# Optimization experiments

Measured on AMD Instinct MI355X. Metric: run time of the kernel, lower is better.

## Reference

```python
import jax, jax.numpy as jnp
import numpy as np

CLOUD_STDS = np.array([0.015, 0.015, 0.015], dtype=np.float32)
D_MODEL = 256
NHEAD = 8
NLAYERS = 4
DFF = 1024
K = 50
TEMP = 10000.0
ORIG_RES = 0.002
ENC_DIM = D_MODEL // 3 // 2  # 42
EPS = 1e-5


def setup_inputs() -> dict:
    key = jax.random.key(0)
    ks = jax.random.split(key, 10)
    B, F, S, d = 2, 8, 512, D_MODEL
    w = lambda k, shape: jax.random.normal(k, shape, jnp.float32) * 0.02
    return {
        "x": jax.random.normal(ks[0], (B, F, S, 3), jnp.float32),
        "is_pad": jnp.zeros((B, F, S), bool),
        "query_embed": w(ks[1], (1, d)),
        "Wq": w(ks[2], (NLAYERS, d, d)), "bq": jnp.zeros((NLAYERS, d), jnp.float32),
        "Wk": w(ks[3], (NLAYERS, d, d)), "bk": jnp.zeros((NLAYERS, d), jnp.float32),
        "Wv": w(ks[4], (NLAYERS, d, d)), "bv": jnp.zeros((NLAYERS, d), jnp.float32),
        "Wo": w(ks[5], (NLAYERS, d, d)), "bo": jnp.zeros((NLAYERS, d), jnp.float32),
        "ln1_g": jnp.ones((NLAYERS, d), jnp.float32), "ln1_b": jnp.zeros((NLAYERS, d), jnp.float32),
        "ln2_g": jnp.ones((NLAYERS, d), jnp.float32), "ln2_b": jnp.zeros((NLAYERS, d), jnp.float32),
        "W1": w(ks[6], (NLAYERS, d, DFF)), "b1": jnp.zeros((NLAYERS, DFF), jnp.float32),
        "W2": w(ks[7], (NLAYERS, DFF, d)), "b2": jnp.zeros((NLAYERS, d), jnp.float32),
    }


def _layer_norm(z, g, b):
    m = z.mean(-1, keepdims=True)
    v = ((z - m) ** 2).mean(-1, keepdims=True)
    return (z - m) / jnp.sqrt(v + EPS) * g + b


def reference(x, is_pad, query_embed, Wq, bq, Wk, bk, Wv, bv, Wo, bo,
              ln1_g, ln1_b, ln2_g, ln2_b, W1, b1, W2, b2):
    bin_size = jnp.asarray(ORIG_RES / CLOUD_STDS)  # (3,)
    B, F, S, _ = x.shape
    d = query_embed.shape[-1]
    H, dh = NHEAD, d // NHEAD
    S1 = S + 1

    def pos_encode(xb):  # (F,S,3) -> (F,S,d)
        xq = jnp.floor(xb / bin_size)  # torch float // == floor division
        dim_t = TEMP ** (jnp.arange(ENC_DIM, dtype=jnp.float32) / ENC_DIM)
        p = xq[..., None] / dim_t  # (F,S,3,E)
        pe = jnp.stack([jnp.sin(p), jnp.cos(p)], axis=-1).reshape(F, S, 3 * ENC_DIM * 2)
        pad = d - 6 * ENC_DIM  # left zero-pad (ZeroPad2d((pad,0,0,0)))
        return jnp.pad(pe, ((0, 0), (0, 0), (pad, 0)))

    def encode_one(xb, pb):  # xb:(F,S,3), pb:(F,S) bool
        # kNN mask: squared dists give same topk-smallest indices as cdist
        d2 = jnp.sum((xb[:, :, None, :] - xb[:, None, :, :]) ** 2, -1)  # (F,S,S)
        _, inds = jax.lax.top_k(-d2, K)  # (F,S,K)
        mask = jnp.ones((F, S1, S1), bool)  # True = disallowed
        fi = jnp.arange(F)[:, None, None]
        ci = jnp.arange(S)[None, :, None]
        mask = mask.at[fi, ci, inds].set(False)
        mask = mask.at[:, -1, :].set(False).at[:, :, -1].set(False)
        key_pad = jnp.concatenate([pb, jnp.zeros((F, 1), bool)], -1)  # (F,S1)
        bias = jnp.where(mask | key_pad[:, None, :], -1e9, 0.0).astype(jnp.float32)[:, None]  # (F,1,S1,S1)

        src = jnp.concatenate([pos_encode(xb), jnp.broadcast_to(query_embed, (F, 1, d))], axis=1)
        scale = 1.0 / jnp.sqrt(jnp.float32(dh))
        for l in range(NLAYERS):  # post-norm TransformerEncoderLayer
            q = (src @ Wq[l] + bq[l]).reshape(F, S1, H, dh)
            k = (src @ Wk[l] + bk[l]).reshape(F, S1, H, dh)
            v = (src @ Wv[l] + bv[l]).reshape(F, S1, H, dh)
            scores = jnp.einsum('fqhd,fkhd->fhqk', q, k) * scale + bias
            attn = jax.nn.softmax(scores, axis=-1)
            o = jnp.einsum('fhqk,fkhd->fqhd', attn, v).reshape(F, S1, d)
            src = _layer_norm(src + o @ Wo[l] + bo[l], ln1_g[l], ln1_b[l])
            ff = jax.nn.relu(src @ W1[l] + b1[l]) @ W2[l] + b2[l]
            src = _layer_norm(src + ff, ln2_g[l], ln2_b[l])
        return src[:, -1]  # query token encoding, (F,d)

    return jax.vmap(encode_one)(x, is_pad)  # (B,F,d)
```

## Files before the change

kernel.cpp:

```cpp
#include <hip/hip_runtime.h>
#include <math.h>

#define D 256
#define SS 512
#define S1 513
#define NC 16
#define NL 4
#define DFF_ 1024
#define NH 8
#define DH 32
#define KNN 50

typedef __attribute__((ext_vector_type(8))) short short8;
typedef __attribute__((ext_vector_type(4))) float float4v;
typedef __attribute__((address_space(1))) const void* gptr_t;
typedef __attribute__((address_space(3))) void* sptr_t;

__device__ __forceinline__ float b2f(short s) {
  return __uint_as_float(((unsigned)(unsigned short)s) << 16);
}
__device__ __forceinline__ short f2b(float f) {
  unsigned u = __float_as_uint(f);
  unsigned r = (u + 0x7fffu + ((u >> 16) & 1u)) >> 16;
  return (short)r;
}
__device__ __forceinline__ int mbcnt64(unsigned long long m) {
  return __builtin_amdgcn_mbcnt_hi((unsigned)(m >> 32),
         __builtin_amdgcn_mbcnt_lo((unsigned)m, 0));
}

__global__ __launch_bounds__(64) void posenc_kernel(const float* __restrict__ x,
    const float* __restrict__ qe, float* __restrict__ src, short* __restrict__ srcb) {
  int c = blockIdx.x, row = blockIdx.y, lane = threadIdx.x;
  size_t ro = ((size_t)c * S1 + row) * D;
  float* out = src + ro;
  short* outb = srcb + ro;
  if (row == SS) {
    for (int i = lane; i < D; i += 64) { float v = qe[i]; out[i] = v; outb[i] = f2b(v); }
    return;
  }
  const float* xp = x + ((size_t)c * SS + row) * 3;
  const float bin = (float)(0.002 / 0.015);
  float xq0 = floorf(xp[0] / bin);
  float xq1 = floorf(xp[1] / bin);
  float xq2 = floorf(xp[2] / bin);
  if (lane < 4) { out[lane] = 0.f; outb[lane] = 0; }
  for (int idx = lane; idx < 126; idx += 64) {
    int ch = idx / 42, e = idx - ch * 42;
    float dimt = powf(10000.0f, (float)e / 42.0f);
    float xq = (ch == 0) ? xq0 : ((ch == 1) ? xq1 : xq2);
    float p = xq / dimt;
    float sv = sinf(p), cv = cosf(p);
    int o0 = 4 + ch * 84 + e * 2;
    out[o0] = sv; out[o0 + 1] = cv;
    outb[o0] = f2b(sv); outb[o0 + 1] = f2b(cv);
  }
}

__global__ __launch_bounds__(64) void knn_kernel(const float* __restrict__ x, int* __restrict__ nbr) {
  int c = blockIdx.x, row = blockIdx.y, lane = threadIdx.x;
  const float* xc = x + (size_t)c * SS * 3;
  float px = xc[row * 3], py = xc[row * 3 + 1], pz = xc[row * 3 + 2];
  unsigned u[8];
  #pragma unroll
  for (int t = 0; t < 8; ++t) {
    int j = lane + 64 * t;
    float dx = px - xc[j * 3], dy = py - xc[j * 3 + 1], dz = pz - xc[j * 3 + 2];
    float s0 = __fmul_rn(dx, dx), s1 = __fmul_rn(dy, dy), s2 = __fmul_rn(dz, dz);
    u[t] = __float_as_uint(__fadd_rn(__fadd_rn(s0, s1), s2));
  }
  unsigned T = 0u;
  #pragma unroll 1
  for (int b = 30; b >= 0; --b) {
    unsigned cand = T | (1u << b);
    int cnt = 0;
    #pragma unroll
    for (int t = 0; t < 8; ++t) cnt += __popcll(__ballot(u[t] < cand));
    if (cnt < KNN) T = cand;
  }
  int L = 0;
  #pragma unroll
  for (int t = 0; t < 8; ++t) L += __popcll(__ballot(u[t] < T));
  int tneed = KNN - L;
  int wbase = 0;
  int* nrow = nbr + ((size_t)c * SS + row) * KNN;
  #pragma unroll
  for (int t = 0; t < 8; ++t) {
    bool less = u[t] < T;
    bool eq = u[t] == T;
    unsigned long long em = __ballot(eq);
    int myeq = mbcnt64(em);
    bool sel = eq && (myeq < tneed);
    bool win = less || sel;
    unsigned long long wm = __ballot(win);
    int mypos = wbase + mbcnt64(wm);
    if (win) nrow[mypos] = lane + 64 * t;
    wbase += __popcll(wm);
    int tie_take = __popcll(em); tie_take = tie_take < tneed ? tie_take : tneed;
    tneed -= tie_take;
  }
}

__global__ __launch_bounds__(256) void wconv4_kernel(const float* __restrict__ Wq,
    const float* __restrict__ Wk, const float* __restrict__ Wv, const float* __restrict__ Wo,
    short* __restrict__ Wqt, short* __restrict__ Wkt, short* __restrict__ Wvt, short* __restrict__ Wot) {
  __shared__ float t[32][33];
  int z = blockIdx.z, which = z >> 2, l = z & 3;
  const float* W = (which == 0 ? Wq : which == 1 ? Wk : which == 2 ? Wv : Wo) + (size_t)l * D * D;
  short* Wt = (which == 0 ? Wqt : which == 1 ? Wkt : which == 2 ? Wvt : Wot) + (size_t)l * D * D;
  int k0 = blockIdx.x * 32, n0 = blockIdx.y * 32;
  int tx = threadIdx.x, ty = threadIdx.y;
  #pragma unroll
  for (int i = 0; i < 4; ++i)
    t[ty + 8 * i][tx] = W[(size_t)(k0 + ty + 8 * i) * D + n0 + tx];
  __syncthreads();
  #pragma unroll
  for (int i = 0; i < 4; ++i)
    Wt[(size_t)(n0 + ty + 8 * i) * D + k0 + tx] = f2b(t[tx][ty + 8 * i]);
}

__global__ __launch_bounds__(256) void wconv_kernel(const float* __restrict__ W,
    short* __restrict__ Wt, int K, int N) {
  __shared__ float t[32][33];
  int m = blockIdx.z;
  const float* Wm = W + (size_t)m * K * N;
  short* Wtm = Wt + (size_t)m * K * N;
  int k0 = blockIdx.x * 32, n0 = blockIdx.y * 32;
  int tx = threadIdx.x, ty = threadIdx.y;
  #pragma unroll
  for (int i = 0; i < 4; ++i)
    t[ty + 8 * i][tx] = Wm[(size_t)(k0 + ty + 8 * i) * N + n0 + tx];
  __syncthreads();
  #pragma unroll
  for (int i = 0; i < 4; ++i)
    Wtm[(size_t)(n0 + ty + 8 * i) * K + k0 + tx] = f2b(t[tx][ty + 8 * i]);
}

template<typename OutT, int RELU>
__global__ __launch_bounds__(256) void mfma_gemm(
    const short* __restrict__ A,
    const short* __restrict__ B0, const short* __restrict__ B1, const short* __restrict__ B2,
    const float* __restrict__ bias0, const float* __restrict__ bias1, const float* __restrict__ bias2,
    OutT* __restrict__ C0, OutT* __restrict__ C1, OutT* __restrict__ C2,
    int M, int N, int Kd) {
  __shared__ short lds[16384];
  const short* Bt  = blockIdx.z == 0 ? B0 : (blockIdx.z == 1 ? B1 : B2);
  const float* bias = blockIdx.z == 0 ? bias0 : (blockIdx.z == 1 ? bias1 : bias2);
  OutT* C          = blockIdx.z == 0 ? C0 : (blockIdx.z == 1 ? C1 : C2);
  int bm = blockIdx.x * 128, bn = blockIdx.y * 128;
  int tid = threadIdx.x, lane = tid & 63, wid = tid >> 6;
  int wr = wid >> 1, wc = wid & 1;
  float4v acc[4][4];
  #pragma unroll
  for (int i = 0; i < 4; ++i)
    #pragma unroll
    for (int j = 0; j < 4; ++j) acc[i][j] = {0.f, 0.f, 0.f, 0.f};

  for (int k0 = 0; k0 < Kd; k0 += 64) {
    #pragma unroll
    for (int q = 0; q < 4; ++q) {
      int row = wid * 32 + q * 8 + (lane >> 3);
      int slot = lane & 7;
      int kofs = k0 + ((slot ^ (row & 7)) << 3);
      {
        int gr = bm + row; if (gr > M - 1) gr = M - 1;
        const short* gp = A + (size_t)gr * Kd + kofs;
        __builtin_amdgcn_global_load_lds((gptr_t)gp, (sptr_t)(&lds[(wid * 32 + q * 8) * 64]), 16, 0, 0);
      }
      {
        const short* gp = Bt + (size_t)(bn + row) * Kd + kofs;
        __builtin_amdgcn_global_load_lds((gptr_t)gp, (sptr_t)(&lds[8192 + (wid * 32 + q * 8) * 64]), 16, 0, 0);
      }
    }
    __syncthreads();
    #pragma unroll
    for (int kh = 0; kh < 2; ++kh) {
      short8 af[4], bf[4];
      int kk = kh * 4 + (lane >> 4);
      #pragma unroll
      for (int i = 0; i < 4; ++i) {
        int row = wr * 64 + i * 16 + (lane & 15);
        af[i] = *(const short8*)&lds[row * 64 + ((kk ^ (row & 7)) << 3)];
      }
      #pragma unroll
      for (int j = 0; j < 4; ++j) {
        int row = wc * 64 + j * 16 + (lane & 15);
        bf[j] = *(const short8*)&lds[8192 + row * 64 + ((kk ^ (row & 7)) << 3)];
      }
      #pragma unroll
      for (int i = 0; i < 4; ++i)
        #pragma unroll
        for (int j = 0; j < 4; ++j)
          acc[i][j] = __builtin_amdgcn_mfma_f32_16x16x32_bf16(af[i], bf[j], acc[i][j], 0, 0, 0);
    }
    __syncthreads();
  }
  #pragma unroll
  for (int i = 0; i < 4; ++i) {
    int gm0 = bm + wr * 64 + i * 16 + ((lane >> 4) << 2);
    #pragma unroll
    for (int j = 0; j < 4; ++j) {
      int gn = bn + wc * 64 + j * 16 + (lane & 15);
      float bsv = bias[gn];
      #pragma unroll
      for (int r = 0; r < 4; ++r) {
        int gm = gm0 + r;
        if (gm < M) {
          float v = acc[i][j][r] + bsv;
          if (RELU) v = fmaxf(v, 0.f);
          if constexpr (sizeof(OutT) == 2) C[(size_t)gm * N + gn] = f2b(v);
          else C[(size_t)gm * N + gn] = v;
        }
      }
    }
  }
}

__global__ __launch_bounds__(256) void gemm_ln(
    const short* __restrict__ A, const short* __restrict__ Bt,
    const float* __restrict__ bias, float* __restrict__ src, short* __restrict__ srcb,
    const float* __restrict__ g, const float* __restrict__ bb, int M, int Kd) {
  __shared__ short ldsA[64 * 64];
  __shared__ short ldsB[256 * 64];
  __shared__ float sBias[256], sG[256], sBb[256];
  int tid = threadIdx.x, lane = tid & 63, wid = tid >> 6;
  int bm = blockIdx.x * 64;
  sBias[tid] = bias[tid]; sG[tid] = g[tid]; sBb[tid] = bb[tid];
  float4v acc[16];
  #pragma unroll
  for (int j = 0; j < 16; ++j) acc[j] = {0.f, 0.f, 0.f, 0.f};

  for (int k0 = 0; k0 < Kd; k0 += 64) {
    int slot = lane & 7;
    #pragma unroll
    for (int q = 0; q < 2; ++q) {
      int row = q * 32 + wid * 8 + (lane >> 3);
      int kofs = k0 + ((slot ^ (row & 7)) << 3);
      int gr = bm + row; if (gr > M - 1) gr = M - 1;
      __builtin_amdgcn_global_load_lds((gptr_t)(A + (size_t)gr * Kd + kofs),
          (sptr_t)(&ldsA[(q * 32 + wid * 8) * 64]), 16, 0, 0);
    }
    #pragma unroll
    for (int q = 0; q < 8; ++q) {
      int row = q * 32 + wid * 8 + (lane >> 3);
      int kofs = k0 + ((slot ^ (row & 7)) << 3);
      __builtin_amdgcn_global_load_lds((gptr_t)(Bt + (size_t)row * Kd + kofs),
          (sptr_t)(&ldsB[(q * 32 + wid * 8) * 64]), 16, 0, 0);
    }
    __syncthreads();
    #pragma unroll
    for (int kh = 0; kh < 2; ++kh) {
      int kk = kh * 4 + (lane >> 4);
      int arow = wid * 16 + (lane & 15);
      short8 af = *(const short8*)&ldsA[arow * 64 + ((kk ^ (arow & 7)) << 3)];
      #pragma unroll
      for (int j = 0; j < 16; ++j) {
        int brow = j * 16 + (lane & 15);
        short8 bf = *(const short8*)&ldsB[brow * 64 + ((kk ^ (brow & 7)) << 3)];
        acc[j] = __builtin_amdgcn_mfma_f32_16x16x32_bf16(af, bf, acc[j], 0, 0, 0);
      }
    }
    __syncthreads();
  }
  int rowg = lane >> 4, coll = lane & 15;
  float z[16][4];
  #pragma unroll
  for (int j = 0; j < 16; ++j) {
    int gn = j * 16 + coll;
    float bsv = sBias[gn];
    #pragma unroll
    for (int r = 0; r < 4; ++r) {
      int gm = bm + wid * 16 + rowg * 4 + r;
      int gmc = gm < M ? gm : M - 1;
      z[j][r] = acc[j][r] + bsv + src[(size_t)gmc * D + gn];
    }
  }
  #pragma unroll
  for (int r = 0; r < 4; ++r) {
    float s = 0.f;
    #pragma unroll
    for (int j = 0; j < 16; ++j) s += z[j][r];
    s += __shfl_xor(s, 1); s += __shfl_xor(s, 2); s += __shfl_xor(s, 4); s += __shfl_xor(s, 8);
    float mean = s * (1.f / 256.f);
    float v = 0.f;
    #pragma unroll
    for (int j = 0; j < 16; ++j) { float d = z[j][r] - mean; v += d * d; }
    v += __shfl_xor(v, 1); v += __shfl_xor(v, 2); v += __shfl_xor(v, 4); v += __shfl_xor(v, 8);
    float scl = rsqrtf(v * (1.f / 256.f) + 1e-5f);
    int gm = bm + wid * 16 + rowg * 4 + r;
    if (gm < M) {
      #pragma unroll
      for (int j = 0; j < 16; ++j) {
        int gn = j * 16 + coll;
        float o = (z[j][r] - mean) * scl * sG[gn] + sBb[gn];
        src[(size_t)gm * D + gn] = o;
        srcb[(size_t)gm * D + gn] = f2b(o);
      }
    }
  }
}

__global__ __launch_bounds__(256) void attn_kernel2(const short* __restrict__ qb,
    const short* __restrict__ kb, const short* __restrict__ vb,
    const int* __restrict__ nbr, short* __restrict__ ob) {
  __shared__ float ps[S1 + 7];
  __shared__ float red[8];
  __shared__ float accp[8][32];
  __shared__ float sum_sh;
  int c = blockIdx.y;
  const float scale = 0.17677669529663687f;

  if (blockIdx.x < 128) {
    int lane = threadIdx.x & 63, w = threadIdx.x >> 6;
    int qrow = blockIdx.x * 4 + w;
    int h = lane >> 3, j = lane & 7;
    const short* cb_k = kb + (size_t)c * S1 * D;
    const short* cb_v = vb + (size_t)c * S1 * D;
    float qv[32];
    {
      const short* qp = qb + ((size_t)c * S1 + qrow) * D + h * DH;
      #pragma unroll
      for (int d8 = 0; d8 < 4; ++d8) {
        short8 q8 = *(const short8*)(qp + d8 * 8);
        #pragma unroll
        for (int e = 0; e < 8; ++e) qv[d8 * 8 + e] = b2f(q8[e]);
      }
    }
    int idxr = SS;
    if (lane < KNN) idxr = nbr[((size_t)c * SS + qrow) * KNN + lane];
    float p[7];
    float mx = -INFINITY;
    #pragma unroll
    for (int c7 = 0; c7 < 7; ++c7) {
      int slot = c7 * 8 + j;
      int is = __shfl(idxr, slot);
      const short* kp = cb_k + (size_t)is * D + h * DH;
      float a = 0.f;
      #pragma unroll
      for (int d8 = 0; d8 < 4; ++d8) {
        short8 k8 = *(const short8*)(kp + d8 * 8);
        #pragma unroll
        for (int e = 0; e < 8; ++e) a += qv[d8 * 8 + e] * b2f(k8[e]);
      }
      p[c7] = (slot < 51) ? a * scale : -INFINITY;
      mx = fmaxf(mx, p[c7]);
    }
    #pragma unroll
    for (int o = 1; o < 8; o <<= 1) mx = fmaxf(mx, __shfl_xor(mx, o));
    float sum = 0.f;
    #pragma unroll
    for (int c7 = 0; c7 < 7; ++c7) { p[c7] = expf(p[c7] - mx); sum += p[c7]; }
    #pragma unroll
    for (int o = 1; o < 8; o <<= 1) sum += __shfl_xor(sum, o);
    float acc0 = 0.f, acc1 = 0.f, acc2 = 0.f, acc3 = 0.f;
    #pragma unroll
    for (int t = 0; t < 51; ++t) {
      float pp = __shfl(p[t >> 3], h * 8 + (t & 7));
      int is = __shfl(idxr, t);
      const short* vp = cb_v + (size_t)is * D + h * DH + j * 4;
      int2 v2 = *(const int2*)vp;
      acc0 += pp * __uint_as_float((unsigned)v2.x << 16);
      acc1 += pp * __uint_as_float((unsigned)v2.x & 0xffff0000u);
      acc2 += pp * __uint_as_float((unsigned)v2.y << 16);
      acc3 += pp * __uint_as_float((unsigned)v2.y & 0xffff0000u);
    }
    float inv = 1.0f / sum;
    short* op = ob + ((size_t)c * S1 + qrow) * D + h * DH + j * 4;
    short4 o4;
    o4.x = f2b(acc0 * inv); o4.y = f2b(acc1 * inv);
    o4.z = f2b(acc2 * inv); o4.w = f2b(acc3 * inv);
    *(short4*)op = o4;
  } else {
    int tid = threadIdx.x, lane = tid & 63, w = tid >> 6;
    int h = blockIdx.x - 128;
    const short* qp = qb + ((size_t)c * S1 + SS) * D + h * DH;
    float qv[32];
    #pragma unroll
    for (int d8 = 0; d8 < 4; ++d8) {
      short8 q8 = *(const short8*)(qp + d8 * 8);
      #pragma unroll
      for (int e = 0; e < 8; ++e) qv[d8 * 8 + e] = b2f(q8[e]);
    }
    float mxl = -INFINITY;
    for (int j = tid; j < S1; j += 256) {
      const short* kp = kb + ((size_t)c * S1 + j) * D + h * DH;
      float a = 0.f;
      #pragma unroll
      for (int d8 = 0; d8 < 4; ++d8) {
        short8 k8 = *(const short8*)(kp + d8 * 8);
        #pragma unroll
        for (int e = 0; e < 8; ++e) a += qv[d8 * 8 + e] * b2f(k8[e]);
      }
      float sc = a * scale;
      ps[j] = sc;
      mxl = fmaxf(mxl, sc);
    }
    #pragma unroll
    for (int o = 32; o > 0; o >>= 1) mxl = fmaxf(mxl, __shfl_xor(mxl, o));
    if (lane == 0) red[w] = mxl;
    __syncthreads();
    float mx = fmaxf(fmaxf(red[0], red[1]), fmaxf(red[2], red[3]));
    float sml = 0.f;
    for (int j = tid; j < S1; j += 256) {
      float p = expf(ps[j] - mx);
      ps[j] = p;
      sml += p;
    }
    #pragma unroll
    for (int o = 32; o > 0; o >>= 1) sml += __shfl_xor(sml, o);
    if (lane == 0) red[4 + w] = sml;
    __syncthreads();
    if (tid == 0) sum_sh = red[4] + red[5] + red[6] + red[7];
    int d = lane & 31;
    int part = w * 2 + (lane >> 5);
    float acc = 0.f;
    __syncthreads();
    for (int j = part; j < S1; j += 8)
      acc += ps[j] * b2f(vb[((size_t)c * S1 + j) * D + h * DH + d]);
    accp[part][d] = acc;
    __syncthreads();
    if (tid < 32) {
      float a = 0.f;
      #pragma unroll
      for (int p8 = 0; p8 < 8; ++p8) a += accp[p8][tid];
      ob[((size_t)c * S1 + SS) * D + h * DH + tid] = f2b(a / sum_sh);
    }
  }
}

__global__ void gather_kernel(const float* __restrict__ src, float* __restrict__ out) {
  int i = blockIdx.x * 256 + threadIdx.x;
  int c = i >> 8, d = i & 255;
  out[i] = src[((size_t)c * S1 + SS) * D + d];
}

extern "C" void kernel_launch(void* const* d_in, const int* in_sizes, int n_in,
                              void* d_out, int out_size, void* d_ws, size_t ws_size,
                              hipStream_t stream) {
  const float* x  = (const float*)d_in[0];
  const float* qe = (const float*)d_in[2];
  const float* Wq = (const float*)d_in[3];
  const float* bq = (const float*)d_in[4];
  const float* Wk = (const float*)d_in[5];
  const float* bk = (const float*)d_in[6];
  const float* Wv = (const float*)d_in[7];
  const float* bv = (const float*)d_in[8];
  const float* Wo = (const float*)d_in[9];
  const float* bo = (const float*)d_in[10];
  const float* ln1_g = (const float*)d_in[11];
  const float* ln1_b = (const float*)d_in[12];
  const float* ln2_g = (const float*)d_in[13];
  const float* ln2_b = (const float*)d_in[14];
  const float* W1 = (const float*)d_in[15];
  const float* b1 = (const float*)d_in[16];
  const float* W2 = (const float*)d_in[17];
  const float* b2 = (const float*)d_in[18];
  float* out = (float*)d_out;

  const size_t SRC_N = (size_t)NC * S1 * D;
  const size_t WSQ   = (size_t)NL * D * D;
  const size_t WFF   = (size_t)NL * D * DFF_;

  float* ws    = (float*)d_ws;
  float* src   = ws;
  short* srcb  = (short*)(src + SRC_N);
  short* big4b = srcb + SRC_N;
  short* qbb   = big4b;
  short* kbb   = qbb + SRC_N;
  short* vbb   = kbb + SRC_N;
  short* attnb = vbb + SRC_N;
  short* ffb   = big4b;
  int*   nbr   = (int*)(big4b + 4 * SRC_N);
  short* Wqt   = (short*)(nbr + (size_t)NC * SS * KNN);
  short* Wkt   = Wqt + WSQ;
  short* Wvt   = Wkt + WSQ;
  short* Wot   = Wvt + WSQ;
  short* W1t   = Wot + WSQ;
  short* W2t   = W1t + WFF;

  const int M = NC * S1;
  const int MB = (M + 127) / 128;
  const int MB64 = (M + 63) / 64;

  wconv4_kernel<<<dim3(8, 8, 16), dim3(32, 8), 0, stream>>>(Wq, Wk, Wv, Wo, Wqt, Wkt, Wvt, Wot);
  wconv_kernel<<<dim3(8, 32, NL), dim3(32, 8), 0, stream>>>(W1, W1t, D, DFF_);
  wconv_kernel<<<dim3(32, 8, NL), dim3(32, 8), 0, stream>>>(W2, W2t, DFF_, D);

  posenc_kernel<<<dim3(NC, S1), 64, 0, stream>>>(x, qe, src, srcb);
  knn_kernel<<<dim3(NC, SS), 64, 0, stream>>>(x, nbr);

  for (int l = 0; l < NL; ++l) {
    const short* Wql = Wqt + (size_t)l * D * D;
    const short* Wkl = Wkt + (size_t)l * D * D;
    const short* Wvl = Wvt + (size_t)l * D * D;
    const short* Wol = Wot + (size_t)l * D * D;
    const short* W1l = W1t + (size_t)l * D * DFF_;
    const short* W2l = W2t + (size_t)l * DFF_ * D;

    mfma_gemm<short, 0><<<dim3(MB, 2, 3), 256, 0, stream>>>(
        srcb, Wql, Wkl, Wvl, bq + l * D, bk + l * D, bv + l * D,
        qbb, kbb, vbb, M, D, D);
    attn_kernel2<<<dim3(136, NC), 256, 0, stream>>>(qbb, kbb, vbb, nbr, attnb);
    gemm_ln<<<MB64, 256, 0, stream>>>(attnb, Wol, bo + l * D, src, srcb,
        ln1_g + l * D, ln1_b + l * D, M, D);
    mfma_gemm<short, 1><<<dim3(MB, 8, 1), 256, 0, stream>>>(
        srcb, W1l, W1l, W1l, b1 + l * DFF_, b1 + l * DFF_, b1 + l * DFF_,
        ffb, ffb, ffb, M, DFF_, D);
    gemm_ln<<<MB64, 256, 0, stream>>>(ffb, W2l, b2 + l * D, src, srcb,
        ln2_g + l * D, ln2_b + l * D, M, DFF_);
  }

  gather_kernel<<<NC, 256, 0, stream>>>(src, out);
}
```

Before: 602.4 us.

## Stage per-head K/V slices in LDS for sparse kNN attention

The kNN attention kernel now stages the full K and V slice for one (cloud, head) pair into shared memory (K padded to a 40-element stride) and serves a block of query rows from it, instead of issuing scattered global gathers for every neighbour. Each wave handles one query at a time, with one lane per neighbour, and uses readlane broadcasts for the probabilities and indices in the PV loop. The global-query rows reuse the same shared buffer. The change trades scattered global and L2 traffic for a large LDS footprint (about 74 KB per block, which limits occupancy), a serial per-query loop, and a grid of 384 blocks.

```diff
diff --git a/kernel.cpp b/kernel.cpp
--- a/kernel.cpp
+++ b/kernel.cpp
@@ -27,6 +27,9 @@
 __device__ __forceinline__ int mbcnt64(unsigned long long m) {
   return __builtin_amdgcn_mbcnt_hi((unsigned)(m >> 32),
          __builtin_amdgcn_mbcnt_lo((unsigned)m, 0));
+}
+__device__ __forceinline__ float readlane_f(float v, int l) {
+  return __uint_as_float(__builtin_amdgcn_readlane(__float_as_uint(v), l));
 }
 
 __global__ __launch_bounds__(64) void posenc_kernel(const float* __restrict__ x,
@@ -300,79 +303,82 @@
   }
 }
 
-__global__ __launch_bounds__(256) void attn_kernel2(const short* __restrict__ qb,
+__global__ __launch_bounds__(256) void attn_lds(const short* __restrict__ qb,
     const short* __restrict__ kb, const short* __restrict__ vb,
     const int* __restrict__ nbr, short* __restrict__ ob) {
-  __shared__ float ps[S1 + 7];
-  __shared__ float red[8];
-  __shared__ float accp[8][32];
-  __shared__ float sum_sh;
-  int c = blockIdx.y;
+  __shared__ __align__(16) short sm[513 * 40 + 513 * 32];
+  short* Kl = sm;
+  short* Vl = sm + 513 * 40;
+  int tid = threadIdx.x, lane = tid & 63, w = tid >> 6;
+  int x = blockIdx.x & 7;
+  int r = blockIdx.x >> 3;
   const float scale = 0.17677669529663687f;
 
-  if (blockIdx.x < 128) {
-    int lane = threadIdx.x & 63, w = threadIdx.x >> 6;
-    int qrow = blockIdx.x * 4 + w;
-    int h = lane >> 3, j = lane & 7;
-    const short* cb_k = kb + (size_t)c * S1 * D;
-    const short* cb_v = vb + (size_t)c * S1 * D;
-    float qv[32];
-    {
-      const short* qp = qb + ((size_t)c * S1 + qrow) * D + h * DH;
+  if (r < 32) {
+    int c = 2 * x + (r >> 4);
+    int h = (r >> 1) & 7;
+    int half = r & 1;
+    const short* kbase = kb + (size_t)c * S1 * D + h * DH;
+    const short* vbase = vb + (size_t)c * S1 * D + h * DH;
+    for (int i = tid; i < 513 * 4; i += 256) {
+      int key = i >> 2, off = (i & 3) * 8;
+      *(int4*)&Kl[key * 40 + off] = *(const int4*)(kbase + (size_t)key * D + off);
+      *(int4*)&Vl[key * 32 + off] = *(const int4*)(vbase + (size_t)key * D + off);
+    }
+    __syncthreads();
+    int qbase = half * 256 + w * 64;
+    #pragma unroll 1
+    for (int qi = 0; qi < 64; ++qi) {
+      int qrow = qbase + qi;
+      int idx = SS;
+      if (lane < KNN) idx = nbr[((size_t)c * SS + qrow) * KNN + lane];
+      const int4* qp = (const int4*)(qb + ((size_t)c * S1 + qrow) * D + h * DH);
+      float qv[32];
       #pragma unroll
       for (int d8 = 0; d8 < 4; ++d8) {
-        short8 q8 = *(const short8*)(qp + d8 * 8);
+        int4 q4 = qp[d8];
+        const unsigned* qw = (const unsigned*)&q4;
         #pragma unroll
-        for (int e = 0; e < 8; ++e) qv[d8 * 8 + e] = b2f(q8[e]);
-      }
-    }
-    int idxr = SS;
-    if (lane < KNN) idxr = nbr[((size_t)c * SS + qrow) * KNN + lane];
-    float p[7];
-    float mx = -INFINITY;
-    #pragma unroll
-    for (int c7 = 0; c7 < 7; ++c7) {
-      int slot = c7 * 8 + j;
-      int is = __shfl(idxr, slot);
-      const short* kp = cb_k + (size_t)is * D + h * DH;
+        for (int w2 = 0; w2 < 4; ++w2) {
+          qv[d8 * 8 + w2 * 2]     = __uint_as_float(qw[w2] << 16);
+          qv[d8 * 8 + w2 * 2 + 1] = __uint_as_float(qw[w2] & 0xffff0000u);
+        }
+      }
       float a = 0.f;
       #pragma unroll
       for (int d8 = 0; d8 < 4; ++d8) {
-        short8 k8 = *(const short8*)(kp + d8 * 8);
+        short8 k8 = *(const short8*)&Kl[idx * 40 + d8 * 8];
         #pragma unroll
         for (int e = 0; e < 8; ++e) a += qv[d8 * 8 + e] * b2f(k8[e]);
       }
-      p[c7] = (slot < 51) ? a * scale : -INFINITY;
-      mx = fmaxf(mx, p[c7]);
-    }
-    #pragma unroll
-    for (int o = 1; o < 8; o <<= 1) mx = fmaxf(mx, __shfl_xor(mx, o));
-    float sum = 0.f;
-    #pragma unroll
-    for (int c7 = 0; c7 < 7; ++c7) { p[c7] = expf(p[c7] - mx); sum += p[c7]; }
-    #pragma unroll
-    for (int o = 1; o < 8; o <<= 1) sum += __shfl_xor(sum, o);
-    float acc0 = 0.f, acc1 = 0.f, acc2 = 0.f, acc3 = 0.f;
-    #pragma unroll
-    for (int t = 0; t < 51; ++t) {
-      float pp = __shfl(p[t >> 3], h * 8 + (t & 7));
-      int is = __shfl(idxr, t);
-      const short* vp = cb_v + (size_t)is * D + h * DH + j * 4;
-      int2 v2 = *(const int2*)vp;
-      acc0 += pp * __uint_as_float((unsigned)v2.x << 16);
-      acc1 += pp * __uint_as_float((unsigned)v2.x & 0xffff0000u);
-      acc2 += pp * __uint_as_float((unsigned)v2.y << 16);
-      acc3 += pp * __uint_as_float((unsigned)v2.y & 0xffff0000u);
-    }
-    float inv = 1.0f / sum;
-    short* op = ob + ((size_t)c * S1 + qrow) * D + h * DH + j * 4;
-    short4 o4;
-    o4.x = f2b(acc0 * inv); o4.y = f2b(acc1 * inv);
-    o4.z = f2b(acc2 * inv); o4.w = f2b(acc3 * inv);
-    *(short4*)op = o4;
+      float sc = (lane <= KNN) ? a * scale : -INFINITY;
+      float mx = sc;
+      #pragma unroll
+      for (int o = 32; o > 0; o >>= 1) mx = fmaxf(mx, __shfl_xor(mx, o));
+      float p = expf(sc - mx);
+      float sum = p;
+      #pragma unroll
+      for (int o = 32; o > 0; o >>= 1) sum += __shfl_xor(sum, o);
+      float inv = 1.0f / sum;
+      int d = lane & 31;
+      float acc = 0.f;
+      #pragma unroll
+      for (int s2 = 0; s2 < 51; ++s2) {
+        float pp = readlane_f(p, s2);
+        int ii = __builtin_amdgcn_readlane(idx, s2);
+        acc += pp * b2f(Vl[ii * 32 + d]);
+      }
+      if (lane < 32)
+        ob[((size_t)c * S1 + qrow) * D + h * DH + d] = f2b(acc * inv);
+    }
   } else {
-    int tid = threadIdx.x, lane = tid & 63, w = tid >> 6;
-    int h = blockIdx.x - 128;
+    int r2 = r - 32;
+    int c = 2 * x + (r2 >> 3);
+    int h = r2 & 7;
+    float* ps = (float*)sm;
+    float* red = ps + 516;
+    float (*accp)[32] = (float(*)[32])(red + 8);
+    float* sum_sh = (float*)(accp + 8);
     const short* qp = qb + ((size_t)c * S1 + SS) * D + h * DH;
     float qv[32];
     #pragma unroll
@@ -410,7 +416,7 @@
     for (int o = 32; o > 0; o >>= 1) sml += __shfl_xor(sml, o);
     if (lane == 0) red[4 + w] = sml;
     __syncthreads();
-    if (tid == 0) sum_sh = red[4] + red[5] + red[6] + red[7];
+    if (tid == 0) *sum_sh = red[4] + red[5] + red[6] + red[7];
     int d = lane & 31;
     int part = w * 2 + (lane >> 5);
     float acc = 0.f;
@@ -423,7 +429,7 @@
       float a = 0.f;
       #pragma unroll
       for (int p8 = 0; p8 < 8; ++p8) a += accp[p8][tid];
-      ob[((size_t)c * S1 + SS) * D + h * DH + tid] = f2b(a / sum_sh);
+      ob[((size_t)c * S1 + SS) * D + h * DH + tid] = f2b(a / *sum_sh);
     }
   }
 }
@@ -500,7 +506,7 @@
     mfma_gemm<short, 0><<<dim3(MB, 2, 3), 256, 0, stream>>>(
         srcb, Wql, Wkl, Wvl, bq + l * D, bk + l * D, bv + l * D,
         qbb, kbb, vbb, M, D, D);
-    attn_kernel2<<<dim3(136, NC), 256, 0, stream>>>(qbb, kbb, vbb, nbr, attnb);
+    attn_lds<<<384, 256, 0, stream>>>(qbb, kbb, vbb, nbr, attnb);
     gemm_ln<<<MB64, 256, 0, stream>>>(attnb, Wol, bo + l * D, src, srcb,
         ln1_g + l * D, ln1_b + l * D, M, D);
     mfma_gemm<short, 1><<<dim3(MB, 8, 1), 256, 0, stream>>>(
```

Result: slower. 861.6 us (+43.0%).
